# Kernel tuning notes

Measured on AMD Instinct MI355X. Metric: run time of the kernel, lower is better.

The kernel has to match this reference:

```python
import jax, jax.numpy as jnp
import numpy as np

L, D, H, E, K, HID = 4096, 1024, 16, 8, 2, 4096
HEAD_DIM = D // H
SCALE = 1.0 / np.sqrt(HEAD_DIM)


def setup_inputs() -> dict:
    key = jax.random.key(0)
    ks = jax.random.split(key, 9)
    s = 0.02
    return {
        "Q": jax.random.normal(ks[0], (L, D), dtype=jnp.float32),
        "K": jax.random.normal(ks[1], (L, D), dtype=jnp.float32),
        "V": jax.random.normal(ks[2], (L, D), dtype=jnp.float32),
        "gate_w": jax.random.normal(ks[3], (D, E), dtype=jnp.float32) * s,
        "w1": jax.random.normal(ks[4], (E, D, HID), dtype=jnp.float32) * s,
        "b1": jnp.zeros((E, HID), dtype=jnp.float32),
        "w2": jax.random.normal(ks[5], (E, HID, D), dtype=jnp.float32) * s,
        "b2": jnp.zeros((E, D), dtype=jnp.float32),
    }


def attention(Q, Kt, V):
    # [L, D] -> [L, H, head_dim]
    q = Q.reshape(L, H, HEAD_DIM)
    k = Kt.reshape(L, H, HEAD_DIM)
    v = V.reshape(L, H, HEAD_DIM)
    scores = jnp.einsum("qhd,khd->hqk", q, k) * SCALE  # [H, L, L]
    probs = jax.nn.softmax(scores, axis=-1)
    out = jnp.einsum("hqk,khd->qhd", probs, v)  # [L, H, head_dim]
    return out.reshape(L, D)


def moe(x, gate_w, w1, b1, w2, b2):
    # x: [N, D]; top-k gating with softmax over selected logits
    logits = x @ gate_w  # [N, E]
    topv, topi = jax.lax.top_k(logits, K)  # [N, K]
    topw = jax.nn.softmax(topv, axis=-1)
    rows = jnp.arange(x.shape[0])[:, None]
    full_w = jnp.zeros_like(logits).at[rows, topi].set(topw)  # [N, E]
    # dense-masked expert compute (mathematically identical: zero weights kill
    # unrouted tokens). GELU is exact (erf), matching torch nn.GELU default.
    h = jax.nn.gelu(jnp.einsum("nd,edh->enh", x, w1) + b1[:, None, :],
                    approximate=False)  # [E, N, HID]
    y = jnp.einsum("enh,ehd->end", h, w2) + b2[:, None, :]  # [E, N, D]
    return jnp.einsum("ne,end->nd", full_w, y)  # weighted combine


def reference(Q, K, V, gate_w, w1, b1, w2, b2):
    attn_out = attention(Q, K, V)              # [L, D]
    out = moe(attn_out, gate_w, w1, b1, w2, b2)  # [L, D]
    return out
```

## Files before the change

### kernel.cpp

```cpp
#include <hip/hip_runtime.h>
#include <hip/hip_bf16.h>
#include <math.h>

#define L_SEQ 4096
#define DMODEL 1024
#define NHEAD 16
#define HDIM 64
#define NEXP 8
#define NHID 4096
#define NSLOT (L_SEQ * 2)

typedef __attribute__((ext_vector_type(4))) float f32x4;
typedef __attribute__((ext_vector_type(8))) short s16x8;
typedef __attribute__((ext_vector_type(4))) short s16x4;

__device__ __forceinline__ short f2bf(float f) {
  __hip_bfloat16 h = __float2bfloat16(f);
  return *reinterpret_cast<short*>(&h);
}
__device__ __forceinline__ float bf2f(short s) {
  __hip_bfloat16 h;
  *reinterpret_cast<short*>(&h) = s;
  return __bfloat162float(h);
}
__device__ __forceinline__ void split3(float a, short& h, short& m, short& l) {
  h = f2bf(a);
  float r = a - bf2f(h);
  m = f2bf(r);
  float r2 = r - bf2f(m);
  l = f2bf(r2);
}
__device__ __forceinline__ void tsplit3(float a, short& h, short& m, short& l) {
  unsigned u = __float_as_uint(a);
  unsigned uh = u & 0xffff0000u;
  float fh = __uint_as_float(uh);
  float r1 = a - fh;
  unsigned um = __float_as_uint(r1) & 0xffff0000u;
  float fm = __uint_as_float(um);
  float r2 = r1 - fm;
  unsigned ul = __float_as_uint(r2) & 0xffff0000u;
  h = (short)(uh >> 16); m = (short)(um >> 16); l = (short)(ul >> 16);
}
__device__ __forceinline__ void gload16(const void* g, void* l) {
  __builtin_amdgcn_global_load_lds(
      (const __attribute__((address_space(1))) void*)g,
      (__attribute__((address_space(3))) void*)l, 16, 0, 0);
}

__global__ __launch_bounds__(256) void split_kernel(const float* __restrict__ src,
                                                    short* __restrict__ hs,
                                                    short* __restrict__ ms,
                                                    short* __restrict__ ls,
                                                    float scale, int nquad) {
  int i = blockIdx.x * 256 + threadIdx.x;
  for (; i < nquad; i += gridDim.x * 256) {
    f32x4 a = reinterpret_cast<const f32x4*>(src)[i];
    a *= scale;
    s16x4 h4, m4, l4;
    #pragma unroll
    for (int j = 0; j < 4; ++j) {
      short h, m, l;
      split3(a[j], h, m, l);
      h4[j] = h; m4[j] = m; l4[j] = l;
    }
    reinterpret_cast<s16x4*>(hs)[i] = h4;
    reinterpret_cast<s16x4*>(ms)[i] = m4;
    reinterpret_cast<s16x4*>(ls)[i] = l4;
  }
}

__global__ __launch_bounds__(256) void split_vt_kernel(const float* __restrict__ V,
                                                       short* __restrict__ Vth,
                                                       short* __restrict__ Vtm,
                                                       short* __restrict__ Vtl) {
  __shared__ float Vlds[64][65];
  const int k0 = blockIdx.x * 64;
  const int head = blockIdx.y;
  const int t = threadIdx.x;
  {
    int r = t >> 2, c = (t & 3) * 16;
    const f32x4* src = reinterpret_cast<const f32x4*>(&V[(size_t)(k0 + r) * DMODEL + head * HDIM + c]);
    #pragma unroll
    for (int j = 0; j < 4; ++j)
      *reinterpret_cast<f32x4*>(&Vlds[r][c + 4 * j]) = src[j];
  }
  __syncthreads();
  {
    int d = t >> 2, kc = (t & 3) * 16;
    s16x8 h8[2], m8[2], l8[2];
    #pragma unroll
    for (int j = 0; j < 16; ++j) {
      float v = Vlds[kc + j][d];
      short h, m, l;
      split3(v, h, m, l);
      h8[j >> 3][j & 7] = h; m8[j >> 3][j & 7] = m; l8[j >> 3][j & 7] = l;
    }
    size_t base = (size_t)(head * HDIM + d) * L_SEQ + k0 + kc;
    *reinterpret_cast<s16x8*>(&Vth[base]) = h8[0];
    *reinterpret_cast<s16x8*>(&Vth[base + 8]) = h8[1];
    *reinterpret_cast<s16x8*>(&Vtm[base]) = m8[0];
    *reinterpret_cast<s16x8*>(&Vtm[base + 8]) = m8[1];
    *reinterpret_cast<s16x8*>(&Vtl[base]) = l8[0];
    *reinterpret_cast<s16x8*>(&Vtl[base + 8]) = l8[1];
  }
}

__global__ __launch_bounds__(256) void wtrans_kernel(const float* __restrict__ src,
                                                     short* __restrict__ dst,
                                                     int R, int C) {
  __shared__ float T[64][65];
  const int e = blockIdx.z;
  const int r0 = blockIdx.y * 64, c0 = blockIdx.x * 64;
  const size_t sbase = (size_t)e * R * C;
  const int t = threadIdx.x;
  {
    int rr = t >> 2, cc = (t & 3) * 16;
    #pragma unroll
    for (int j = 0; j < 4; ++j)
      *reinterpret_cast<f32x4*>(&T[rr][cc + 4 * j]) =
          *reinterpret_cast<const f32x4*>(&src[sbase + (size_t)(r0 + rr) * C + c0 + cc + 4 * j]);
  }
  __syncthreads();
  {
    int c = t >> 2, r = (t & 3) * 16;
    s16x8 v0, v1;
    #pragma unroll
    for (int j = 0; j < 8; ++j) { v0[j] = f2bf(T[r + j][c]); v1[j] = f2bf(T[r + 8 + j][c]); }
    size_t dbase = ((size_t)e * C + c0 + c) * R + r0 + r;
    *reinterpret_cast<s16x8*>(&dst[dbase]) = v0;
    *reinterpret_cast<s16x8*>(&dst[dbase + 8]) = v1;
  }
}

__global__ __launch_bounds__(256) void attn_mfma(
    const short* __restrict__ Qh, const short* __restrict__ Qm, const short* __restrict__ Ql,
    const short* __restrict__ Kh, const short* __restrict__ Km, const short* __restrict__ Kl,
    const short* __restrict__ Vth, const short* __restrict__ Vtm, const short* __restrict__ Vtl,
    float* __restrict__ X) {
  __shared__ short Ks[3][64][68];
  __shared__ short Vs[3][64][68];
  __shared__ short Ps[4][3][16][68];
  const int lin = blockIdx.x;
  const int swz = (lin & 7) * 128 + (lin >> 3);
  const int head = swz >> 6;
  const int q0 = (swz & 63) << 6;
  const int t = threadIdx.x;
  const int lane = t & 63;
  const int wq = t >> 6;
  const int lq = lane & 15;
  const int lg = lane >> 4;

  const short* Qp[3] = {Qh, Qm, Ql};
  const short* Kp[3] = {Kh, Km, Kl};
  const short* Vp[3] = {Vth, Vtm, Vtl};

  s16x8 qf[3][2];
  {
    size_t qrow = (size_t)(q0 + wq * 16 + lq) * DMODEL + head * HDIM;
    #pragma unroll
    for (int s = 0; s < 3; ++s)
      #pragma unroll
      for (int dc = 0; dc < 2; ++dc)
        qf[s][dc] = *reinterpret_cast<const s16x8*>(&Qp[s][qrow + dc * 32 + lg * 8]);
  }

  s16x8 sK[3][2], sV[3][2];
  const int c0 = t * 2;
  const int row0 = c0 >> 3, ch0 = (c0 & 7) * 8;
  const int row1 = (c0 + 1) >> 3, ch1 = ((c0 + 1) & 7) * 8;

  #define LOAD_TILE(k0v)                                                                  \
    _Pragma("unroll")                                                                     \
    for (int s = 0; s < 3; ++s) {                                                         \
      sK[s][0] = *reinterpret_cast<const s16x8*>(&Kp[s][(size_t)((k0v) + row0) * DMODEL + head * HDIM + ch0]); \
      sK[s][1] = *reinterpret_cast<const s16x8*>(&Kp[s][(size_t)((k0v) + row1) * DMODEL + head * HDIM + ch1]); \
      sV[s][0] = *reinterpret_cast<const s16x8*>(&Vp[s][(size_t)(head * HDIM + row0) * L_SEQ + (k0v) + ch0]);  \
      sV[s][1] = *reinterpret_cast<const s16x8*>(&Vp[s][(size_t)(head * HDIM + row1) * L_SEQ + (k0v) + ch1]);  \
    }

  f32x4 acc[4];
  #pragma unroll
  for (int dt = 0; dt < 4; ++dt) acc[dt] = (f32x4)0.f;
  float l_run = 0.f;
  const float LOG2E = 1.4426950408889634f;
  const float MBIAS = 46.166241f;

  LOAD_TILE(0);

  for (int kt64 = 0; kt64 < 64; ++kt64) {
    __syncthreads();
    #pragma unroll
    for (int s = 0; s < 3; ++s) {
      *reinterpret_cast<s16x8*>(&Ks[s][row0][ch0]) = sK[s][0];
      *reinterpret_cast<s16x8*>(&Ks[s][row1][ch1]) = sK[s][1];
      *reinterpret_cast<s16x8*>(&Vs[s][row0][ch0]) = sV[s][0];
      *reinterpret_cast<s16x8*>(&Vs[s][row1][ch1]) = sV[s][1];
    }
    __syncthreads();
    if (kt64 < 63) { LOAD_TILE((kt64 + 1) * 64); }

    f32x4 st[4];
    #pragma unroll
    for (int kt = 0; kt < 4; ++kt) {
      st[kt] = (f32x4)0.f;
      #pragma unroll
      for (int dc = 0; dc < 2; ++dc) {
        s16x8 ah = *reinterpret_cast<const s16x8*>(&Ks[0][kt * 16 + lq][dc * 32 + lg * 8]);
        s16x8 am = *reinterpret_cast<const s16x8*>(&Ks[1][kt * 16 + lq][dc * 32 + lg * 8]);
        s16x8 al = *reinterpret_cast<const s16x8*>(&Ks[2][kt * 16 + lq][dc * 32 + lg * 8]);
        st[kt] = __builtin_amdgcn_mfma_f32_16x16x32_bf16(am, qf[1][dc], st[kt], 0, 0, 0);
        st[kt] = __builtin_amdgcn_mfma_f32_16x16x32_bf16(al, qf[0][dc], st[kt], 0, 0, 0);
        st[kt] = __builtin_amdgcn_mfma_f32_16x16x32_bf16(ah, qf[2][dc], st[kt], 0, 0, 0);
        st[kt] = __builtin_amdgcn_mfma_f32_16x16x32_bf16(am, qf[0][dc], st[kt], 0, 0, 0);
        st[kt] = __builtin_amdgcn_mfma_f32_16x16x32_bf16(ah, qf[1][dc], st[kt], 0, 0, 0);
        st[kt] = __builtin_amdgcn_mfma_f32_16x16x32_bf16(ah, qf[0][dc], st[kt], 0, 0, 0);
      }
    }

    float psum = 0.f;
    #pragma unroll
    for (int kt = 0; kt < 4; ++kt) {
      s16x4 h4, m4, l4;
      #pragma unroll
      for (int r = 0; r < 4; ++r) {
        float p = exp2f(fmaf(st[kt][r], LOG2E, -MBIAS));
        psum += p;
        short h, m, l;
        tsplit3(p, h, m, l);
        h4[r] = h; m4[r] = m; l4[r] = l;
      }
      int kcol = kt * 16 + lg * 4;
      *reinterpret_cast<s16x4*>(&Ps[wq][0][lq][kcol]) = h4;
      *reinterpret_cast<s16x4*>(&Ps[wq][1][lq][kcol]) = m4;
      *reinterpret_cast<s16x4*>(&Ps[wq][2][lq][kcol]) = l4;
    }
    psum += __shfl_xor(psum, 16);
    psum += __shfl_xor(psum, 32);
    l_run += psum;

    #pragma unroll
    for (int kc = 0; kc < 2; ++kc) {
      s16x8 ph = *reinterpret_cast<const s16x8*>(&Ps[wq][0][lq][kc * 32 + lg * 8]);
      s16x8 pm = *reinterpret_cast<const s16x8*>(&Ps[wq][1][lq][kc * 32 + lg * 8]);
      s16x8 pl = *reinterpret_cast<const s16x8*>(&Ps[wq][2][lq][kc * 32 + lg * 8]);
      #pragma unroll
      for (int dt = 0; dt < 4; ++dt) {
        s16x8 vh = *reinterpret_cast<const s16x8*>(&Vs[0][dt * 16 + lq][kc * 32 + lg * 8]);
        s16x8 vm = *reinterpret_cast<const s16x8*>(&Vs[1][dt * 16 + lq][kc * 32 + lg * 8]);
        s16x8 vl = *reinterpret_cast<const s16x8*>(&Vs[2][dt * 16 + lq][kc * 32 + lg * 8]);
        acc[dt] = __builtin_amdgcn_mfma_f32_16x16x32_bf16(pm, vm, acc[dt], 0, 0, 0);
        acc[dt] = __builtin_amdgcn_mfma_f32_16x16x32_bf16(pl, vh, acc[dt], 0, 0, 0);
        acc[dt] = __builtin_amdgcn_mfma_f32_16x16x32_bf16(ph, vl, acc[dt], 0, 0, 0);
        acc[dt] = __builtin_amdgcn_mfma_f32_16x16x32_bf16(pm, vh, acc[dt], 0, 0, 0);
        acc[dt] = __builtin_amdgcn_mfma_f32_16x16x32_bf16(ph, vm, acc[dt], 0, 0, 0);
        acc[dt] = __builtin_amdgcn_mfma_f32_16x16x32_bf16(ph, vh, acc[dt], 0, 0, 0);
      }
    }
  }

  float inv = 1.f / l_run;
  float inv_r[4];
  #pragma unroll
  for (int r = 0; r < 4; ++r) {
    int src = (lg * 4 + r) << 2;
    inv_r[r] = __int_as_float(__builtin_amdgcn_ds_bpermute(src, __float_as_int(inv)));
  }
  #pragma unroll
  for (int dt = 0; dt < 4; ++dt)
    #pragma unroll
    for (int r = 0; r < 4; ++r)
      X[(size_t)(q0 + wq * 16 + lg * 4 + r) * DMODEL + head * HDIM + dt * 16 + lq] = acc[dt][r] * inv_r[r];
}

__global__ __launch_bounds__(256) void tobf16_kernel(const float* __restrict__ src,
                                                     short* __restrict__ dst, int n8) {
  int i = blockIdx.x * 256 + threadIdx.x;
  if (i >= n8) return;
  const f32x4* s = reinterpret_cast<const f32x4*>(src) + (size_t)i * 2;
  f32x4 a = s[0], b = s[1];
  s16x8 r;
  #pragma unroll
  for (int j = 0; j < 4; ++j) { r[j] = f2bf(a[j]); r[4 + j] = f2bf(b[j]); }
  reinterpret_cast<s16x8*>(dst)[i] = r;
}

__global__ __launch_bounds__(256) void gate_kernel(const float* __restrict__ X,
                                                   const float* __restrict__ GW,
                                                   int* __restrict__ tokE,
                                                   float* __restrict__ tokW,
                                                   int* __restrict__ meta) {
  const int gid = blockIdx.x * 256 + threadIdx.x;
  const int n = gid >> 6;
  const int lane = threadIdx.x & 63;
  double lacc[8];
  #pragma unroll
  for (int e = 0; e < 8; ++e) lacc[e] = 0.0;
  #pragma unroll
  for (int ch = 0; ch < 4; ++ch) {
    int d0 = ch * 256 + lane * 4;
    f32x4 xv = *reinterpret_cast<const f32x4*>(&X[(size_t)n * DMODEL + d0]);
    #pragma unroll
    for (int j = 0; j < 4; ++j) {
      const f32x4* g = reinterpret_cast<const f32x4*>(&GW[(size_t)(d0 + j) * 8]);
      f32x4 g0 = g[0], g1 = g[1];
      double xd = (double)xv[j];
      lacc[0] += xd * (double)g0[0]; lacc[1] += xd * (double)g0[1];
      lacc[2] += xd * (double)g0[2]; lacc[3] += xd * (double)g0[3];
      lacc[4] += xd * (double)g1[0]; lacc[5] += xd * (double)g1[1];
      lacc[6] += xd * (double)g1[2]; lacc[7] += xd * (double)g1[3];
    }
  }
  #pragma unroll
  for (int e = 0; e < 8; ++e) {
    double v = lacc[e];
    #pragma unroll
    for (int off = 32; off > 0; off >>= 1) v += __shfl_down(v, off);
    lacc[e] = v;
  }
  if (lane == 0) {
    float lg[8];
    #pragma unroll
    for (int e = 0; e < 8; ++e) lg[e] = (float)lacc[e];
    int i0 = 0;
    for (int e = 1; e < 8; ++e) if (lg[e] > lg[i0]) i0 = e;
    int i1 = -1;
    for (int e = 0; e < 8; ++e) {
      if (e == i0) continue;
      if (i1 < 0 || lg[e] > lg[i1]) i1 = e;
    }
    float eb = expf(lg[i1] - lg[i0]);
    float wa = 1.f / (1.f + eb);
    float wb = eb * wa;
    tokE[2 * n] = i0; tokE[2 * n + 1] = i1;
    tokW[2 * n] = wa; tokW[2 * n + 1] = wb;
    atomicAdd(&meta[i0], 1);
    atomicAdd(&meta[i1], 1);
  }
}

__global__ void scan_kernel(int* meta) {
  if (threadIdx.x == 0) {
    int s = 0;
    for (int e = 0; e < 8; ++e) { meta[8 + e] = s; meta[16 + e] = s; s += meta[e]; }
  }
}

__global__ __launch_bounds__(256) void assign_kernel(const int* __restrict__ tokE,
                                                     const float* __restrict__ tokW,
                                                     int* __restrict__ meta,
                                                     int* __restrict__ list,
                                                     float* __restrict__ wl) {
  int n = blockIdx.x * 256 + threadIdx.x;
  if (n >= L_SEQ) return;
  #pragma unroll
  for (int k2 = 0; k2 < 2; ++k2) {
    int e = tokE[2 * n + k2];
    int slot = atomicAdd(&meta[16 + e], 1);
    list[slot] = n;
    wl[slot] = tokW[2 * n + k2];
  }
}

__global__ __launch_bounds__(256) void gemm1p_kernel(const short* __restrict__ Xb,
                                                     const short* __restrict__ W1t,
                                                     const float* __restrict__ B1,
                                                     const int* __restrict__ meta,
                                                     const int* __restrict__ list,
                                                     short* __restrict__ Hb) {
  const int e = blockIdx.z;
  const int cntE = meta[e];
  const int flat = blockIdx.x + gridDim.x * blockIdx.y;
  const int xcd = flat & 7;
  const int idx = flat >> 3;
  const int m0 = (idx & 31) << 7;
  const int n0 = ((xcd << 2) + (idx >> 5)) << 7;
  if (m0 >= cntE) return;
  const int baseE = meta[8 + e];

  __shared__ short As[2][128 * 64];
  __shared__ short Bs[2][128 * 64];

  const int t = threadIdx.x;
  const int l = t & 63;
  const int w = t >> 6;
  const int wm = w >> 1, wn = w & 1;
  const int ln = l & 15, kg = l >> 4;

  size_t asrc[4], bsrc[4];
  #pragma unroll
  for (int c = 0; c < 4; ++c) {
    int row = c * 32 + w * 8 + (l >> 3);
    int idxm = m0 + row; if (idxm > cntE - 1) idxm = cntE - 1;
    int grow = list[baseE + idxm];
    int sch = (l & 7) ^ (row & 7);
    asrc[c] = ((size_t)grow * DMODEL + sch * 8) * 2;
    bsrc[c] = (((size_t)e * NHID + n0 + row) * DMODEL + sch * 8) * 2;
  }

  f32x4 acc[4][4];
  #pragma unroll
  for (int mi = 0; mi < 4; ++mi)
    #pragma unroll
    for (int ni = 0; ni < 4; ++ni) acc[mi][ni] = (f32x4)0.f;

  #define STAGE1(buf, ktv) do {                                                     \
    size_t koff = (size_t)(ktv) * 128;                                              \
    _Pragma("unroll")                                                               \
    for (int c = 0; c < 4; ++c) {                                                   \
      gload16((const char*)Xb + asrc[c] + koff, (char*)As + (buf) * 16384 + c * 4096 + w * 1024);  \
      gload16((const char*)W1t + bsrc[c] + koff, (char*)Bs + (buf) * 16384 + c * 4096 + w * 1024); \
    } } while (0)

  STAGE1(0, 0);
  __syncthreads();
  int cur = 0;
  for (int kt = 0; kt < 16; ++kt) {
    if (kt < 15) STAGE1(cur ^ 1, kt + 1);
    #pragma unroll
    for (int dc = 0; dc < 2; ++dc) {
      s16x8 af[4];
      #pragma unroll
      for (int mi = 0; mi < 4; ++mi) {
        int row = wm * 64 + mi * 16 + ln;
        int c = (dc * 4 + kg) ^ (row & 7);
        af[mi] = *reinterpret_cast<const s16x8*>((char*)As + cur * 16384 + row * 128 + c * 16);
      }
      #pragma unroll
      for (int ni = 0; ni < 4; ++ni) {
        int col = wn * 64 + ni * 16 + ln;
        int c = (dc * 4 + kg) ^ (col & 7);
        s16x8 bfr = *reinterpret_cast<const s16x8*>((char*)Bs + cur * 16384 + col * 128 + c * 16);
        #pragma unroll
        for (int mi = 0; mi < 4; ++mi)
          acc[mi][ni] = __builtin_amdgcn_mfma_f32_16x16x32_bf16(af[mi], bfr, acc[mi][ni], 0, 0, 0);
      }
    }
    __syncthreads();
    cur ^= 1;
  }

  #pragma unroll
  for (int mi = 0; mi < 4; ++mi) {
    #pragma unroll
    for (int r = 0; r < 4; ++r) {
      int rl = wm * 64 + mi * 16 + kg * 4 + r;
      if (m0 + rl >= cntE) continue;
      size_t hrow = (size_t)(baseE + m0 + rl) * NHID;
      #pragma unroll
      for (int ni = 0; ni < 4; ++ni) {
        int col = n0 + wn * 64 + ni * 16 + ln;
        float z = acc[mi][ni][r] + B1[e * NHID + col];
        float g = 0.5f * z * (1.f + erff(z * 0.70710678118f));
        Hb[hrow + col] = f2bf(g);
      }
    }
  }
}

__global__ __launch_bounds__(256) void gemm2p_kernel(const short* __restrict__ Hb,
                                                     const short* __restrict__ W2t,
                                                     const float* __restrict__ B2,
                                                     const int* __restrict__ meta,
                                                     const int* __restrict__ list,
                                                     const float* __restrict__ wl,
                                                     float* __restrict__ out) {
  const int e = blockIdx.z;
  const int cntE = meta[e];
  const int flat = blockIdx.x + gridDim.x * blockIdx.y;
  const int m0 = (flat >> 3) << 7;
  const int n0 = (flat & 7) << 7;
  if (m0 >= cntE) return;
  const int baseE = meta[8 + e];

  __shared__ short As[2][128 * 64];
  __shared__ short Bs[2][128 * 64];

  const int t = threadIdx.x;
  const int l = t & 63;
  const int w = t >> 6;
  const int wm = w >> 1, wn = w & 1;
  const int ln = l & 15, kg = l >> 4;

  size_t asrc[4], bsrc[4];
  #pragma unroll
  for (int c = 0; c < 4; ++c) {
    int row = c * 32 + w * 8 + (l >> 3);
    int idxm = m0 + row; if (idxm > cntE - 1) idxm = cntE - 1;
    int sch = (l & 7) ^ (row & 7);
    asrc[c] = (((size_t)(baseE + idxm)) * NHID + sch * 8) * 2;
    bsrc[c] = (((size_t)e * DMODEL + n0 + row) * NHID + sch * 8) * 2;
  }

  f32x4 acc[4][4];
  #pragma unroll
  for (int mi = 0; mi < 4; ++mi)
    #pragma unroll
    for (int ni = 0; ni < 4; ++ni) acc[mi][ni] = (f32x4)0.f;

  #define STAGE2(buf, ktv) do {                                                     \
    size_t koff = (size_t)(ktv) * 128;                                              \
    _Pragma("unroll")                                                               \
    for (int c = 0; c < 4; ++c) {                                                   \
      gload16((const char*)Hb + asrc[c] + koff, (char*)As + (buf) * 16384 + c * 4096 + w * 1024);  \
      gload16((const char*)W2t + bsrc[c] + koff, (char*)Bs + (buf) * 16384 + c * 4096 + w * 1024); \
    } } while (0)

  STAGE2(0, 0);
  __syncthreads();
  int cur = 0;
  for (int kt = 0; kt < 64; ++kt) {
    if (kt < 63) STAGE2(cur ^ 1, kt + 1);
    #pragma unroll
    for (int dc = 0; dc < 2; ++dc) {
      s16x8 af[4];
      #pragma unroll
      for (int mi = 0; mi < 4; ++mi) {
        int row = wm * 64 + mi * 16 + ln;
        int c = (dc * 4 + kg) ^ (row & 7);
        af[mi] = *reinterpret_cast<const s16x8*>((char*)As + cur * 16384 + row * 128 + c * 16);
      }
      #pragma unroll
      for (int ni = 0; ni < 4; ++ni) {
        int col = wn * 64 + ni * 16 + ln;
        int c = (dc * 4 + kg) ^ (col & 7);
        s16x8 bfr = *reinterpret_cast<const s16x8*>((char*)Bs + cur * 16384 + col * 128 + c * 16);
        #pragma unroll
        for (int mi = 0; mi < 4; ++mi)
          acc[mi][ni] = __builtin_amdgcn_mfma_f32_16x16x32_bf16(af[mi], bfr, acc[mi][ni], 0, 0, 0);
      }
    }
    __syncthreads();
    cur ^= 1;
  }

  #pragma unroll
  for (int mi = 0; mi < 4; ++mi) {
    #pragma unroll
    for (int r = 0; r < 4; ++r) {
      int rl = wm * 64 + mi * 16 + kg * 4 + r;
      if (m0 + rl >= cntE) continue;
      int slot = baseE + m0 + rl;
      int token = list[slot];
      float wgt = wl[slot];
      #pragma unroll
      for (int ni = 0; ni < 4; ++ni) {
        int col = n0 + wn * 64 + ni * 16 + ln;
        float z = acc[mi][ni][r] + B2[e * DMODEL + col];
        atomicAdd(&out[(size_t)token * DMODEL + col], wgt * z);
      }
    }
  }
}

extern "C" void kernel_launch(void* const* d_in, const int* in_sizes, int n_in,
                              void* d_out, int out_size, void* d_ws, size_t ws_size,
                              hipStream_t stream) {
  const float* Q  = (const float*)d_in[0];
  const float* K  = (const float*)d_in[1];
  const float* V  = (const float*)d_in[2];
  const float* GW = (const float*)d_in[3];
  const float* W1 = (const float*)d_in[4];
  const float* B1 = (const float*)d_in[5];
  const float* W2 = (const float*)d_in[6];
  const float* B2 = (const float*)d_in[7];
  float* out = (float*)d_out;

  const size_t SPLIT = (size_t)L_SEQ * DMODEL;
  const size_t WT_BYTES = (size_t)NEXP * NHID * DMODEL * 2;
  const size_t SPLIT_REGION = SPLIT * 2 * 9;
  const size_t SMALL = (size_t)L_SEQ * 2 * 4 * 2 + (size_t)NSLOT * 4 * 2 + 256;
  const size_t PRIMARY_BYTES = WT_BYTES * 2 + SPLIT_REGION + SPLIT * 4 + SMALL;
  if (ws_size < PRIMARY_BYTES) return;

  char* ws = (char*)d_ws;
  const int nquad = (int)(SPLIT / 4);

  size_t off = 0;
  short* W1t = (short*)(ws + off); off += WT_BYTES;
  short* W2t = (short*)(ws + off); off += WT_BYTES;
  char*  splits = ws + off;        off += SPLIT_REGION;
  short* Qh = (short*)(splits);
  short* Qm = Qh + SPLIT;  short* Ql = Qm + SPLIT;
  short* Kh = Ql + SPLIT;  short* Km = Kh + SPLIT;  short* Kl = Km + SPLIT;
  short* Vth = Kl + SPLIT; short* Vtm = Vth + SPLIT; short* Vtl = Vtm + SPLIT;
  short* Hb = (short*)splits;
  short* Xb = (short*)(splits + (size_t)NSLOT * NHID * 2);
  float* Xf = (float*)(ws + off);  off += SPLIT * 4;
  int*   tokE = (int*)(ws + off);  off += (size_t)L_SEQ * 2 * 4;
  float* tokW = (float*)(ws + off); off += (size_t)L_SEQ * 2 * 4;
  int*   list = (int*)(ws + off);  off += (size_t)NSLOT * 4;
  float* wl = (float*)(ws + off);  off += (size_t)NSLOT * 4;
  int*   meta = (int*)(ws + off);  off += 256;

  hipMemsetAsync(out, 0, (size_t)out_size * sizeof(float), stream);
  hipMemsetAsync(meta, 0, 256, stream);

  wtrans_kernel<<<dim3(64, 16, 8), 256, 0, stream>>>(W1, W1t, DMODEL, NHID);
  wtrans_kernel<<<dim3(16, 64, 8), 256, 0, stream>>>(W2, W2t, NHID, DMODEL);
  split_kernel<<<dim3(2048), 256, 0, stream>>>(Q, Qh, Qm, Ql, 0.125f, nquad);
  split_kernel<<<dim3(2048), 256, 0, stream>>>(K, Kh, Km, Kl, 1.0f, nquad);
  split_vt_kernel<<<dim3(64, 16), 256, 0, stream>>>(V, Vth, Vtm, Vtl);
  attn_mfma<<<dim3(1024), 256, 0, stream>>>(Qh, Qm, Ql, Kh, Km, Kl, Vth, Vtm, Vtl, Xf);
  tobf16_kernel<<<dim3(2048), 256, 0, stream>>>(Xf, Xb, (int)(SPLIT / 8));
  gate_kernel<<<dim3(1024), 256, 0, stream>>>(Xf, GW, tokE, tokW, meta);
  scan_kernel<<<1, 64, 0, stream>>>(meta);
  assign_kernel<<<dim3(16), 256, 0, stream>>>(tokE, tokW, meta, list, wl);
  gemm1p_kernel<<<dim3(32, 32, 8), 256, 0, stream>>>(Xb, W1t, B1, meta, list, Hb);
  gemm2p_kernel<<<dim3(32, 8, 8), 256, 0, stream>>>(Hb, W2t, B2, meta, list, wl, out);
}
```

Baseline: 1.097 ms.

## Switch attention to 32x32x16 MFMA with register-level P exchange

Rewrites the attention kernel to use 32x32x16 bf16 MFMA instead of 16x16x32. Each wave now owns 32 query rows, so each block covers 128 queries and half as many blocks are launched. The split probabilities move from the score accumulator layout to the A-operand layout through cross-lane shuffles, which removes the LDS round-trip for P. The K/V LDS padding changes and launch bounds ask for 2 blocks per CU. The aim is higher MFMA efficiency and less LDS traffic, at the cost of more register pressure and fewer blocks to spread across the GPU.

```diff
diff --git a/kernel.cpp b/kernel.cpp
--- a/kernel.cpp
+++ b/kernel.cpp
@@ -11,8 +11,10 @@
 #define NSLOT (L_SEQ * 2)
 
 typedef __attribute__((ext_vector_type(4))) float f32x4;
+typedef __attribute__((ext_vector_type(16))) float f32x16;
 typedef __attribute__((ext_vector_type(8))) short s16x8;
 typedef __attribute__((ext_vector_type(4))) short s16x4;
+typedef __attribute__((ext_vector_type(4))) unsigned u32x4;
 
 __device__ __forceinline__ short f2bf(float f) {
   __hip_bfloat16 h = __float2bfloat16(f);
@@ -29,17 +31,6 @@
   m = f2bf(r);
   float r2 = r - bf2f(m);
   l = f2bf(r2);
-}
-__device__ __forceinline__ void tsplit3(float a, short& h, short& m, short& l) {
-  unsigned u = __float_as_uint(a);
-  unsigned uh = u & 0xffff0000u;
-  float fh = __uint_as_float(uh);
-  float r1 = a - fh;
-  unsigned um = __float_as_uint(r1) & 0xffff0000u;
-  float fm = __uint_as_float(um);
-  float r2 = r1 - fm;
-  unsigned ul = __float_as_uint(r2) & 0xffff0000u;
-  h = (short)(uh >> 16); m = (short)(um >> 16); l = (short)(ul >> 16);
 }
 __device__ __forceinline__ void gload16(const void* g, void* l) {
   __builtin_amdgcn_global_load_lds(
@@ -132,36 +123,35 @@
   }
 }
 
-__global__ __launch_bounds__(256) void attn_mfma(
+__global__ __launch_bounds__(256, 2) void attn_mfma(
     const short* __restrict__ Qh, const short* __restrict__ Qm, const short* __restrict__ Ql,
     const short* __restrict__ Kh, const short* __restrict__ Km, const short* __restrict__ Kl,
     const short* __restrict__ Vth, const short* __restrict__ Vtm, const short* __restrict__ Vtl,
     float* __restrict__ X) {
-  __shared__ short Ks[3][64][68];
-  __shared__ short Vs[3][64][68];
-  __shared__ short Ps[4][3][16][68];
+  __shared__ short Ks[3][64][70];
+  __shared__ short Vs[3][64][70];
   const int lin = blockIdx.x;
-  const int swz = (lin & 7) * 128 + (lin >> 3);
-  const int head = swz >> 6;
-  const int q0 = (swz & 63) << 6;
+  const int swz = (lin & 7) * 64 + (lin >> 3);
+  const int head = swz >> 5;
+  const int q0 = (swz & 31) << 7;
   const int t = threadIdx.x;
-  const int lane = t & 63;
+  const int l = t & 63;
   const int wq = t >> 6;
-  const int lq = lane & 15;
-  const int lg = lane >> 4;
+  const int lc = l & 31;
+  const int hh = l >> 5;
 
   const short* Qp[3] = {Qh, Qm, Ql};
   const short* Kp[3] = {Kh, Km, Kl};
   const short* Vp[3] = {Vth, Vtm, Vtl};
 
-  s16x8 qf[3][2];
+  s16x8 qf[3][4];
   {
-    size_t qrow = (size_t)(q0 + wq * 16 + lq) * DMODEL + head * HDIM;
+    size_t qrow = (size_t)(q0 + wq * 32 + lc) * DMODEL + head * HDIM;
     #pragma unroll
     for (int s = 0; s < 3; ++s)
       #pragma unroll
-      for (int dc = 0; dc < 2; ++dc)
-        qf[s][dc] = *reinterpret_cast<const s16x8*>(&Qp[s][qrow + dc * 32 + lg * 8]);
+      for (int ds_ = 0; ds_ < 4; ++ds_)
+        qf[s][ds_] = *reinterpret_cast<const s16x8*>(&Qp[s][qrow + ds_ * 16 + hh * 8]);
   }
 
   s16x8 sK[3][2], sV[3][2];
@@ -178,10 +168,8 @@
       sV[s][1] = *reinterpret_cast<const s16x8*>(&Vp[s][(size_t)(head * HDIM + row1) * L_SEQ + (k0v) + ch1]);  \
     }
 
-  f32x4 acc[4];
-  #pragma unroll
-  for (int dt = 0; dt < 4; ++dt) acc[dt] = (f32x4)0.f;
-  float l_run = 0.f;
+  f32x16 acc0 = (f32x16)0.f, acc1 = (f32x16)0.f;
+  float l_loc = 0.f;
   const float LOG2E = 1.4426950408889634f;
   const float MBIAS = 46.166241f;
 
@@ -199,77 +187,96 @@
     __syncthreads();
     if (kt64 < 63) { LOAD_TILE((kt64 + 1) * 64); }
 
-    f32x4 st[4];
-    #pragma unroll
-    for (int kt = 0; kt < 4; ++kt) {
-      st[kt] = (f32x4)0.f;
-      #pragma unroll
-      for (int dc = 0; dc < 2; ++dc) {
-        s16x8 ah = *reinterpret_cast<const s16x8*>(&Ks[0][kt * 16 + lq][dc * 32 + lg * 8]);
-        s16x8 am = *reinterpret_cast<const s16x8*>(&Ks[1][kt * 16 + lq][dc * 32 + lg * 8]);
-        s16x8 al = *reinterpret_cast<const s16x8*>(&Ks[2][kt * 16 + lq][dc * 32 + lg * 8]);
-        st[kt] = __builtin_amdgcn_mfma_f32_16x16x32_bf16(am, qf[1][dc], st[kt], 0, 0, 0);
-        st[kt] = __builtin_amdgcn_mfma_f32_16x16x32_bf16(al, qf[0][dc], st[kt], 0, 0, 0);
-        st[kt] = __builtin_amdgcn_mfma_f32_16x16x32_bf16(ah, qf[2][dc], st[kt], 0, 0, 0);
-        st[kt] = __builtin_amdgcn_mfma_f32_16x16x32_bf16(am, qf[0][dc], st[kt], 0, 0, 0);
-        st[kt] = __builtin_amdgcn_mfma_f32_16x16x32_bf16(ah, qf[1][dc], st[kt], 0, 0, 0);
-        st[kt] = __builtin_amdgcn_mfma_f32_16x16x32_bf16(ah, qf[0][dc], st[kt], 0, 0, 0);
-      }
-    }
-
-    float psum = 0.f;
-    #pragma unroll
-    for (int kt = 0; kt < 4; ++kt) {
-      s16x4 h4, m4, l4;
-      #pragma unroll
-      for (int r = 0; r < 4; ++r) {
-        float p = exp2f(fmaf(st[kt][r], LOG2E, -MBIAS));
-        psum += p;
-        short h, m, l;
-        tsplit3(p, h, m, l);
-        h4[r] = h; m4[r] = m; l4[r] = l;
-      }
-      int kcol = kt * 16 + lg * 4;
-      *reinterpret_cast<s16x4*>(&Ps[wq][0][lq][kcol]) = h4;
-      *reinterpret_cast<s16x4*>(&Ps[wq][1][lq][kcol]) = m4;
-      *reinterpret_cast<s16x4*>(&Ps[wq][2][lq][kcol]) = l4;
-    }
-    psum += __shfl_xor(psum, 16);
-    psum += __shfl_xor(psum, 32);
-    l_run += psum;
-
-    #pragma unroll
-    for (int kc = 0; kc < 2; ++kc) {
-      s16x8 ph = *reinterpret_cast<const s16x8*>(&Ps[wq][0][lq][kc * 32 + lg * 8]);
-      s16x8 pm = *reinterpret_cast<const s16x8*>(&Ps[wq][1][lq][kc * 32 + lg * 8]);
-      s16x8 pl = *reinterpret_cast<const s16x8*>(&Ps[wq][2][lq][kc * 32 + lg * 8]);
-      #pragma unroll
-      for (int dt = 0; dt < 4; ++dt) {
-        s16x8 vh = *reinterpret_cast<const s16x8*>(&Vs[0][dt * 16 + lq][kc * 32 + lg * 8]);
-        s16x8 vm = *reinterpret_cast<const s16x8*>(&Vs[1][dt * 16 + lq][kc * 32 + lg * 8]);
-        s16x8 vl = *reinterpret_cast<const s16x8*>(&Vs[2][dt * 16 + lq][kc * 32 + lg * 8]);
-        acc[dt] = __builtin_amdgcn_mfma_f32_16x16x32_bf16(pm, vm, acc[dt], 0, 0, 0);
-        acc[dt] = __builtin_amdgcn_mfma_f32_16x16x32_bf16(pl, vh, acc[dt], 0, 0, 0);
-        acc[dt] = __builtin_amdgcn_mfma_f32_16x16x32_bf16(ph, vl, acc[dt], 0, 0, 0);
-        acc[dt] = __builtin_amdgcn_mfma_f32_16x16x32_bf16(pm, vh, acc[dt], 0, 0, 0);
-        acc[dt] = __builtin_amdgcn_mfma_f32_16x16x32_bf16(ph, vm, acc[dt], 0, 0, 0);
-        acc[dt] = __builtin_amdgcn_mfma_f32_16x16x32_bf16(ph, vh, acc[dt], 0, 0, 0);
-      }
-    }
-  }
-
-  float inv = 1.f / l_run;
-  float inv_r[4];
-  #pragma unroll
-  for (int r = 0; r < 4; ++r) {
-    int src = (lg * 4 + r) << 2;
-    inv_r[r] = __int_as_float(__builtin_amdgcn_ds_bpermute(src, __float_as_int(inv)));
-  }
-  #pragma unroll
-  for (int dt = 0; dt < 4; ++dt)
-    #pragma unroll
-    for (int r = 0; r < 4; ++r)
-      X[(size_t)(q0 + wq * 16 + lg * 4 + r) * DMODEL + head * HDIM + dt * 16 + lq] = acc[dt][r] * inv_r[r];
+    #pragma unroll
+    for (int khalf = 0; khalf < 2; ++khalf) {
+      f32x16 st = (f32x16)0.f;
+      #pragma unroll
+      for (int ds_ = 0; ds_ < 4; ++ds_) {
+        s16x8 ah = *reinterpret_cast<const s16x8*>(&Ks[0][khalf * 32 + lc][ds_ * 16 + hh * 8]);
+        s16x8 am = *reinterpret_cast<const s16x8*>(&Ks[1][khalf * 32 + lc][ds_ * 16 + hh * 8]);
+        s16x8 al = *reinterpret_cast<const s16x8*>(&Ks[2][khalf * 32 + lc][ds_ * 16 + hh * 8]);
+        st = __builtin_amdgcn_mfma_f32_32x32x16_bf16(am, qf[1][ds_], st, 0, 0, 0);
+        st = __builtin_amdgcn_mfma_f32_32x32x16_bf16(al, qf[0][ds_], st, 0, 0, 0);
+        st = __builtin_amdgcn_mfma_f32_32x32x16_bf16(ah, qf[2][ds_], st, 0, 0, 0);
+        st = __builtin_amdgcn_mfma_f32_32x32x16_bf16(am, qf[0][ds_], st, 0, 0, 0);
+        st = __builtin_amdgcn_mfma_f32_32x32x16_bf16(ah, qf[1][ds_], st, 0, 0, 0);
+        st = __builtin_amdgcn_mfma_f32_32x32x16_bf16(ah, qf[0][ds_], st, 0, 0, 0);
+      }
+
+      unsigned Eh[4][2], Em[4][2], El[4][2];
+      float ps = 0.f;
+      #pragma unroll
+      for (int q = 0; q < 4; ++q) {
+        #pragma unroll
+        for (int p = 0; p < 2; ++p) {
+          float a = exp2f(fmaf(st[4 * q + 2 * p],     LOG2E, -MBIAS));
+          float b = exp2f(fmaf(st[4 * q + 2 * p + 1], LOG2E, -MBIAS));
+          ps += a + b;
+          unsigned ua = __float_as_uint(a), ub = __float_as_uint(b);
+          unsigned ha = ua & 0xffff0000u, hb = ub & 0xffff0000u;
+          Eh[q][p] = (ha >> 16) | hb;
+          float ra = a - __uint_as_float(ha), rb = b - __uint_as_float(hb);
+          unsigned ma = __float_as_uint(ra) & 0xffff0000u, mb = __float_as_uint(rb) & 0xffff0000u;
+          Em[q][p] = (ma >> 16) | mb;
+          float la = ra - __uint_as_float(ma), lb = rb - __uint_as_float(mb);
+          El[q][p] = ((__float_as_uint(la) & 0xffff0000u) >> 16) | (__float_as_uint(lb) & 0xffff0000u);
+        }
+      }
+      l_loc += ps;
+
+      #define EXCH(E, Fout) do { u32x4 f_;                                        \
+        _Pragma("unroll") for (int p_ = 0; p_ < 2; ++p_) {                        \
+          unsigned sel_ = hh ? E[2 * ks][p_] : E[2 * ks + 1][p_];                 \
+          unsigned rc_ = (unsigned)__shfl_xor((int)sel_, 32);                     \
+          f_[p_] = hh ? rc_ : E[2 * ks][p_];                                      \
+          f_[2 + p_] = hh ? E[2 * ks + 1][p_] : rc_;                              \
+        }                                                                         \
+        Fout = *reinterpret_cast<s16x8*>(&f_); } while (0)
+
+      #pragma unroll
+      for (int ks = 0; ks < 2; ++ks) {
+        s16x8 Fh, Fm, Fl;
+        EXCH(Eh, Fh);
+        EXCH(Em, Fm);
+        EXCH(El, Fl);
+        const int kcol = khalf * 32 + ks * 16 + hh * 8;
+        {
+          s16x8 vh = *reinterpret_cast<const s16x8*>(&Vs[0][lc][kcol]);
+          s16x8 vm = *reinterpret_cast<const s16x8*>(&Vs[1][lc][kcol]);
+          s16x8 vl = *reinterpret_cast<const s16x8*>(&Vs[2][lc][kcol]);
+          acc0 = __builtin_amdgcn_mfma_f32_32x32x16_bf16(Fm, vm, acc0, 0, 0, 0);
+          acc0 = __builtin_amdgcn_mfma_f32_32x32x16_bf16(Fl, vh, acc0, 0, 0, 0);
+          acc0 = __builtin_amdgcn_mfma_f32_32x32x16_bf16(Fh, vl, acc0, 0, 0, 0);
+          acc0 = __builtin_amdgcn_mfma_f32_32x32x16_bf16(Fm, vh, acc0, 0, 0, 0);
+          acc0 = __builtin_amdgcn_mfma_f32_32x32x16_bf16(Fh, vm, acc0, 0, 0, 0);
+          acc0 = __builtin_amdgcn_mfma_f32_32x32x16_bf16(Fh, vh, acc0, 0, 0, 0);
+        }
+        {
+          s16x8 vh = *reinterpret_cast<const s16x8*>(&Vs[0][32 + lc][kcol]);
+          s16x8 vm = *reinterpret_cast<const s16x8*>(&Vs[1][32 + lc][kcol]);
+          s16x8 vl = *reinterpret_cast<const s16x8*>(&Vs[2][32 + lc][kcol]);
+          acc1 = __builtin_amdgcn_mfma_f32_32x32x16_bf16(Fm, vm, acc1, 0, 0, 0);
+          acc1 = __builtin_amdgcn_mfma_f32_32x32x16_bf16(Fl, vh, acc1, 0, 0, 0);
+          acc1 = __builtin_amdgcn_mfma_f32_32x32x16_bf16(Fh, vl, acc1, 0, 0, 0);
+          acc1 = __builtin_amdgcn_mfma_f32_32x32x16_bf16(Fm, vh, acc1, 0, 0, 0);
+          acc1 = __builtin_amdgcn_mfma_f32_32x32x16_bf16(Fh, vm, acc1, 0, 0, 0);
+          acc1 = __builtin_amdgcn_mfma_f32_32x32x16_bf16(Fh, vh, acc1, 0, 0, 0);
+        }
+      }
+      #undef EXCH
+    }
+  }
+
+  float l_tot = l_loc + __shfl_xor(l_loc, 32);
+  float inv = 1.f / l_tot;
+  #pragma unroll
+  for (int r = 0; r < 16; ++r) {
+    int qrow_ = (r & 3) + 8 * (r >> 2) + 4 * hh;
+    float invr = __int_as_float(__builtin_amdgcn_ds_bpermute(qrow_ << 2, __float_as_int(inv)));
+    size_t base = (size_t)(q0 + wq * 32 + qrow_) * DMODEL + head * HDIM + lc;
+    X[base] = acc0[r] * invr;
+    X[base + 32] = acc1[r] * invr;
+  }
 }
 
 __global__ __launch_bounds__(256) void tobf16_kernel(const float* __restrict__ src,
@@ -600,7 +607,7 @@
   split_kernel<<<dim3(2048), 256, 0, stream>>>(Q, Qh, Qm, Ql, 0.125f, nquad);
   split_kernel<<<dim3(2048), 256, 0, stream>>>(K, Kh, Km, Kl, 1.0f, nquad);
   split_vt_kernel<<<dim3(64, 16), 256, 0, stream>>>(V, Vth, Vtm, Vtl);
-  attn_mfma<<<dim3(1024), 256, 0, stream>>>(Qh, Qm, Ql, Kh, Km, Kl, Vth, Vtm, Vtl, Xf);
+  attn_mfma<<<dim3(512), 256, 0, stream>>>(Qh, Qm, Ql, Kh, Km, Kl, Vth, Vtm, Vtl, Xf);
   tobf16_kernel<<<dim3(2048), 256, 0, stream>>>(Xf, Xb, (int)(SPLIT / 8));
   gate_kernel<<<dim3(1024), 256, 0, stream>>>(Xf, GW, tokE, tokW, meta);
   scan_kernel<<<1, 64, 0, stream>>>(meta);
```

New measurement: 1.069 ms. -2.5%, faster.
